# Kernel optimization log

Measured on AMD Instinct MI355X. Metric: run time of the kernel, lower is better.

The kernel has to match this reference:

```python
import jax, jax.numpy as jnp
import numpy as np

B, N, C, H = 2, 2048, 1024, 16
D = C // H  # head_dim = 64
EPS = 1e-6


def rmsnorm(x, w, eps=EPS):
    # RMSNorm over last dim (head_dim), matching torch RMSNorm (computed in fp32)
    x32 = x.astype(jnp.float32)
    y = x32 * jax.lax.rsqrt(jnp.mean(x32 * x32, axis=-1, keepdims=True) + eps)
    return y.astype(x.dtype) * w


def setup_inputs() -> dict:
    key = jax.random.key(0)
    ks = jax.random.split(key, 4)
    return {
        "x": jax.random.normal(ks[0], (B, N, C), dtype=jnp.float32),
        "w_qkv": jax.random.normal(ks[1], (C, 3 * C), dtype=jnp.float32) * 0.02,
        "b_qkv": jnp.zeros((3 * C,), dtype=jnp.float32),
        "q_w": jnp.ones((D,), dtype=jnp.float32),
        "k_w": jnp.ones((D,), dtype=jnp.float32),
        "w_proj": jax.random.normal(ks[2], (C, C), dtype=jnp.float32) * 0.02,
        "b_proj": jnp.zeros((C,), dtype=jnp.float32),
    }


def reference(x, w_qkv, b_qkv, q_w, k_w, w_proj, b_proj):
    b, n, c = x.shape
    h, d = H, c // H
    # QKV projection -> [3, B, H, N, D]
    qkv = (x @ w_qkv + b_qkv).reshape(b, n, 3, h, d).transpose(2, 0, 3, 1, 4)
    q, k, v = qkv[0], qkv[1], qkv[2]
    # per-head RMSNorm on q/k (qk_norm=True, use_rmsnorm=True)
    q = rmsnorm(q, q_w)
    k = rmsnorm(k, k_w)
    # scaled dot-product attention (scale = head_dim**-0.5, no dropout at eval)
    scale = d ** -0.5
    attn = jax.nn.softmax(jnp.einsum('bhqd,bhkd->bhqk', q, k) * scale, axis=-1)
    out = jnp.einsum('bhqk,bhkd->bhqd', attn, v)  # [B,H,N,D]
    out = out.transpose(0, 2, 1, 3).reshape(b, n, c)
    return out @ w_proj + b_proj
```

## Files before the change

### kernel.cpp

```cpp
#include <hip/hip_runtime.h>

typedef unsigned short u16;
typedef unsigned int u32;
typedef float f4 __attribute__((ext_vector_type(4)));
typedef __bf16 b8 __attribute__((ext_vector_type(8)));
typedef _Float16 h4 __attribute__((ext_vector_type(4)));
typedef _Float16 h8 __attribute__((ext_vector_type(8)));
typedef __fp16 hp2 __attribute__((ext_vector_type(2)));

#if __has_builtin(__builtin_amdgcn_exp2f)
#define EXP2(x) __builtin_amdgcn_exp2f(x)
#else
#define EXP2(x) exp2f(x)
#endif

__device__ __forceinline__ u16 f2bf(float f) {
  unsigned u = __float_as_uint(f);
  u += 0x7fffu + ((u >> 16) & 1u);
  return (u16)(u >> 16);
}
__device__ __forceinline__ float bf2f(u16 h) {
  return __uint_as_float(((unsigned)h) << 16);
}

__global__ void k_convert_all(const float* __restrict__ x,
                              const float* __restrict__ w_qkv,
                              const float* __restrict__ w_proj,
                              u16* __restrict__ xb, u16* __restrict__ wqkT,
                              u16* __restrict__ wpjT) {
  __shared__ u16 t[64][65];
  int bid = blockIdx.x;
  if (bid < 2048) {
    int i = (bid * 256 + threadIdx.x) * 8;
    float4 a = *(const float4*)(x + i);
    float4 b = *(const float4*)(x + i + 4);
    union { u16 h[8]; uint4 v; } r;
    r.h[0] = f2bf(a.x); r.h[1] = f2bf(a.y); r.h[2] = f2bf(a.z); r.h[3] = f2bf(a.w);
    r.h[4] = f2bf(b.x); r.h[5] = f2bf(b.y); r.h[6] = f2bf(b.z); r.h[7] = f2bf(b.w);
    *(uint4*)(xb + i) = r.v;
    return;
  }
  const float* w; u16* wT; int Ncols, Krows, bx, by;
  if (bid < 2816) { int l = bid - 2048; w = w_qkv; wT = wqkT; Ncols = 3072; Krows = 1024; bx = l % 48; by = l / 48; }
  else            { int l = bid - 2816; w = w_proj; wT = wpjT; Ncols = 1024; Krows = 1024; bx = l & 15; by = l >> 4; }
  int n0 = bx * 64, k0 = by * 64;
#pragma unroll
  for (int it = 0; it < 4; ++it) {
    int e = it * 256 + threadIdx.x;
    int r = e >> 4, c0 = (e & 15) * 4;
    float4 v = *(const float4*)(w + (size_t)(k0 + r) * Ncols + n0 + c0);
    t[r][c0] = f2bf(v.x); t[r][c0 + 1] = f2bf(v.y);
    t[r][c0 + 2] = f2bf(v.z); t[r][c0 + 3] = f2bf(v.w);
  }
  __syncthreads();
#pragma unroll
  for (int it = 0; it < 4; ++it) {
    int e = it * 256 + threadIdx.x;
    int r = e >> 4, c0 = (e & 15) * 4;
    union { u16 h[4]; uint2 v; } pk;
    pk.h[0] = t[c0][r]; pk.h[1] = t[c0 + 1][r];
    pk.h[2] = t[c0 + 2][r]; pk.h[3] = t[c0 + 3][r];
    *(uint2*)(wT + (size_t)(n0 + r) * Krows + k0 + c0) = pk.v;
  }
}

__global__ __launch_bounds__(512, 2) void k_gemm_qkv(
    const u16* __restrict__ A, const u16* __restrict__ Bt,
    const float* __restrict__ bias,
    u16* __restrict__ oq, u16* __restrict__ ok, u16* __restrict__ ov,
    const float* __restrict__ qw, const float* __restrict__ kw,
    int K) {
  __shared__ u16 lA[2][256 * 32];
  __shared__ u16 lB[2][256 * 32];
  const int tid = threadIdx.x;
  const int lane = tid & 63, lrow = lane & 15, lq = lane >> 4;
  const int wave = tid >> 6;
  const int bm = blockIdx.y * 256, bn = blockIdx.x * 256;
  const int wm = (wave >> 2) * 128;
  const int wn = (wave & 3) * 64;

  const int ch0 = tid, ch1 = 512 + tid;
  const u16* ap0 = A + (size_t)(bm + (ch0 >> 2)) * K + (ch0 & 3) * 8;
  const u16* ap1 = A + (size_t)(bm + (ch1 >> 2)) * K + (ch1 & 3) * 8;
  const u16* bp0 = Bt + (size_t)(bn + (ch0 >> 2)) * K + (ch0 & 3) * 8;
  const u16* bp1 = Bt + (size_t)(bn + (ch1 >> 2)) * K + (ch1 & 3) * 8;

  uint4 pA0 = *(const uint4*)ap0, pA1 = *(const uint4*)ap1;
  uint4 pB0 = *(const uint4*)bp0, pB1 = *(const uint4*)bp1;

  f4 acc[8][4] = {};
  const int iters = K >> 5;
  for (int it = 0; it < iters; ++it) {
    const int s = it & 1;
    *(uint4*)(lA[s] + ch0 * 8) = pA0; *(uint4*)(lA[s] + ch1 * 8) = pA1;
    *(uint4*)(lB[s] + ch0 * 8) = pB0; *(uint4*)(lB[s] + ch1 * 8) = pB1;
    if (it + 1 < iters) {
      ap0 += 32; ap1 += 32; bp0 += 32; bp1 += 32;
      pA0 = *(const uint4*)ap0; pA1 = *(const uint4*)ap1;
      pB0 = *(const uint4*)bp0; pB1 = *(const uint4*)bp1;
    }
    __syncthreads();
    b8 af[8], bf[4];
#pragma unroll
    for (int i = 0; i < 8; ++i)
      af[i] = *(const b8*)(lA[s] + (wm + i * 16 + lrow) * 32 + lq * 8);
#pragma unroll
    for (int j = 0; j < 4; ++j)
      bf[j] = *(const b8*)(lB[s] + (wn + j * 16 + lrow) * 32 + lq * 8);
#pragma unroll
    for (int i = 0; i < 8; ++i)
#pragma unroll
      for (int j = 0; j < 4; ++j)
        acc[i][j] = __builtin_amdgcn_mfma_f32_16x16x32_bf16(af[i], bf[j], acc[i][j], 0, 0, 0);
  }

  float bv[4];
#pragma unroll
  for (int j = 0; j < 4; ++j) bv[j] = bias[bn + wn + j * 16 + lrow];

  const float CS = 0.125f * 1.44269504088896340736f;
  const int n0w = bn + wn;
  const int sec = n0w >> 10;
  const int h = (n0w >> 6) & 15;
#pragma unroll
  for (int i = 0; i < 8; ++i) {
    float v[4][4];
#pragma unroll
    for (int j = 0; j < 4; ++j)
#pragma unroll
      for (int r = 0; r < 4; ++r) v[j][r] = acc[i][j][r] + bv[j];
    if (sec < 2) {
      u16* dst = sec == 0 ? oq : ok;
      const float* w = sec == 0 ? qw : kw;
      float ex = sec == 0 ? CS : 1.0f;
#pragma unroll
      for (int r = 0; r < 4; ++r) {
        float ss = v[0][r] * v[0][r] + v[1][r] * v[1][r] +
                   v[2][r] * v[2][r] + v[3][r] * v[3][r];
        ss += __shfl_xor(ss, 1, 64); ss += __shfl_xor(ss, 2, 64);
        ss += __shfl_xor(ss, 4, 64); ss += __shfl_xor(ss, 8, 64);
        float sc = rsqrtf(ss * (1.0f / 64.0f) + 1e-6f) * ex;
        int m = bm + wm + i * 16 + lq * 4 + r;
        int bb = m >> 11, ns = m & 2047;
        u16* rowp = dst + ((size_t)(bb * 16 + h) * 2048 + ns) * 64;
#pragma unroll
        for (int j = 0; j < 4; ++j) {
          int d = j * 16 + lrow;
          rowp[d] = f2bf(v[j][r] * sc * w[d]);
        }
      }
    } else {
      int m0 = bm + wm + i * 16 + lq * 4;
      int bb = m0 >> 11, ns = m0 & 2047;
#pragma unroll
      for (int j = 0; j < 4; ++j) {
        int d = j * 16 + lrow;
        union { _Float16 hh[4]; uint2 u; } pk;
#pragma unroll
        for (int r = 0; r < 4; ++r) pk.hh[r] = (_Float16)v[j][r];
        *(uint2*)(ov + ((size_t)(bb * 16 + h) * 64 + d) * 2048 + ns) = pk.u;
      }
    }
  }
}

__global__ __launch_bounds__(256, 4) void k_gemm2(
    const u16* __restrict__ A, const u16* __restrict__ Bt,
    const float* __restrict__ bias, float* __restrict__ outF,
    int K, int Ncols) {
  __shared__ u16 lA[2][64 * 32];
  __shared__ u16 lB[2][128 * 32];
  const int tid = threadIdx.x;
  const int lane = tid & 63, lrow = lane & 15, lq = lane >> 4;
  const int wave = tid >> 6;
  const int bm = blockIdx.y * 64, bn = blockIdx.x * 128;
  const int wm = (wave >> 1) * 32, wn = (wave & 1) * 64;

  const int cha = tid;
  const int ch0 = tid, ch1 = 256 + tid;
  const u16* ap = A + (size_t)(bm + (cha >> 2)) * K + (cha & 3) * 8;
  const u16* bp0 = Bt + (size_t)(bn + (ch0 >> 2)) * K + (ch0 & 3) * 8;
  const u16* bp1 = Bt + (size_t)(bn + (ch1 >> 2)) * K + (ch1 & 3) * 8;

  uint4 pA = *(const uint4*)ap;
  uint4 pB0 = *(const uint4*)bp0, pB1 = *(const uint4*)bp1;

  f4 acc[2][4] = {};
  const int iters = K >> 5;
  for (int it = 0; it < iters; ++it) {
    const int s = it & 1;
    *(uint4*)(lA[s] + cha * 8) = pA;
    *(uint4*)(lB[s] + ch0 * 8) = pB0; *(uint4*)(lB[s] + ch1 * 8) = pB1;
    if (it + 1 < iters) {
      ap += 32; bp0 += 32; bp1 += 32;
      pA = *(const uint4*)ap;
      pB0 = *(const uint4*)bp0; pB1 = *(const uint4*)bp1;
    }
    __syncthreads();
    b8 af[2], bf[4];
#pragma unroll
    for (int i = 0; i < 2; ++i)
      af[i] = *(const b8*)(lA[s] + (wm + i * 16 + lrow) * 32 + lq * 8);
#pragma unroll
    for (int j = 0; j < 4; ++j)
      bf[j] = *(const b8*)(lB[s] + (wn + j * 16 + lrow) * 32 + lq * 8);
#pragma unroll
    for (int i = 0; i < 2; ++i)
#pragma unroll
      for (int j = 0; j < 4; ++j)
        acc[i][j] = __builtin_amdgcn_mfma_f32_16x16x32_bf16(af[i], bf[j], acc[i][j], 0, 0, 0);
  }
#pragma unroll
  for (int i = 0; i < 2; ++i)
#pragma unroll
    for (int j = 0; j < 4; ++j) {
      int n = bn + wn + j * 16 + lrow;
      float bv = bias[n];
#pragma unroll
      for (int r = 0; r < 4; ++r) {
        int m = bm + wm + i * 16 + lq * 4 + r;
        outF[(size_t)m * Ncols + n] = acc[i][j][r] + bv;
      }
    }
}

__global__ __launch_bounds__(512, 2) void k_attn(
    const u16* __restrict__ qb, const u16* __restrict__ kb,
    const u16* __restrict__ vt, u16* __restrict__ ao) {
  __shared__ u16 lK[2][128 * 72];
  __shared__ u16 lV[2][64 * 140];
  const int b = blockIdx.x;
  const int bh = b & 31;
  const int q0 = (b >> 5) * 256;
  const int tid = threadIdx.x, wave = tid >> 6, lane = tid & 63;
  const int lrow = lane & 15, lq = lane >> 4;
  const int wq = wave * 32;

  b8 qf[2][2];
#pragma unroll
  for (int g = 0; g < 2; ++g)
#pragma unroll
    for (int ks = 0; ks < 2; ++ks)
      qf[g][ks] = *(const b8*)(qb + ((size_t)bh * 2048 + q0 + wq + g * 16 + lrow) * 64 +
                               ks * 32 + lq * 8);

  f4 o[2][4] = {};
  f4 lsum[2] = {};

  const int ch0 = tid, ch1 = 512 + tid;
  const u16* kp0 = kb + (size_t)bh * 2048 * 64 + (size_t)(ch0 >> 3) * 64 + (ch0 & 7) * 8;
  const u16* kp1 = kb + (size_t)bh * 2048 * 64 + (size_t)(ch1 >> 3) * 64 + (ch1 & 7) * 8;
  const u16* vp0 = vt + (size_t)bh * 64 * 2048 + (size_t)(ch0 >> 4) * 2048 + (ch0 & 15) * 8;
  const u16* vp1 = vt + (size_t)bh * 64 * 2048 + (size_t)(ch1 >> 4) * 2048 + (ch1 & 15) * 8;
  const int kO0 = (ch0 >> 3) * 72 + (ch0 & 7) * 8;
  const int kO1 = (ch1 >> 3) * 72 + (ch1 & 7) * 8;
  const int vO0 = (ch0 >> 4) * 140 + (ch0 & 15) * 8;
  const int vO1 = (ch1 >> 4) * 140 + (ch1 & 15) * 8;

  uint4 pK0 = *(const uint4*)kp0, pK1 = *(const uint4*)kp1;
  uint4 pV0 = *(const uint4*)vp0, pV1 = *(const uint4*)vp1;

  for (int it = 0; it < 16; ++it) {
    const int s = it & 1;
    *(uint4*)(lK[s] + kO0) = pK0;
    *(uint4*)(lK[s] + kO1) = pK1;
    *(uint2*)(lV[s] + vO0) = make_uint2(pV0.x, pV0.y);
    *(uint2*)(lV[s] + vO0 + 4) = make_uint2(pV0.z, pV0.w);
    *(uint2*)(lV[s] + vO1) = make_uint2(pV1.x, pV1.y);
    *(uint2*)(lV[s] + vO1 + 4) = make_uint2(pV1.z, pV1.w);

    if (it < 15) {
      kp0 += 128 * 64; kp1 += 128 * 64; vp0 += 128; vp1 += 128;
      pK0 = *(const uint4*)kp0; pK1 = *(const uint4*)kp1;
      pV0 = *(const uint4*)vp0; pV1 = *(const uint4*)vp1;
    }
    __syncthreads();

#pragma unroll
    for (int c = 0; c < 4; ++c) {
      f4 st[2][2] = {};
      __builtin_amdgcn_s_setprio(1);
#pragma unroll
      for (int ks = 0; ks < 2; ++ks)
#pragma unroll
        for (int t = 0; t < 2; ++t) {
          b8 kf = *(const b8*)(lK[s] + ((c * 2 + t) * 16 + lrow) * 72 + ks * 32 + lq * 8);
          st[0][t] = __builtin_amdgcn_mfma_f32_16x16x32_bf16(kf, qf[0][ks], st[0][t], 0, 0, 0);
          st[1][t] = __builtin_amdgcn_mfma_f32_16x16x32_bf16(kf, qf[1][ks], st[1][t], 0, 0, 0);
        }
      __builtin_amdgcn_s_setprio(0);

      h8 pf[2];
#pragma unroll
      for (int g = 0; g < 2; ++g) {
        f4 eA, eB;
#pragma unroll
        for (int r = 0; r < 4; ++r) eA[r] = EXP2(st[g][0][r]);
#pragma unroll
        for (int r = 0; r < 4; ++r) eB[r] = EXP2(st[g][1][r]);
        lsum[g] += eA;
        lsum[g] += eB;
        union { hp2 p2[4]; h8 v; } cv;
        cv.p2[0] = __builtin_amdgcn_cvt_pkrtz(eA[0], eA[1]);
        cv.p2[1] = __builtin_amdgcn_cvt_pkrtz(eA[2], eA[3]);
        cv.p2[2] = __builtin_amdgcn_cvt_pkrtz(eB[0], eB[1]);
        cv.p2[3] = __builtin_amdgcn_cvt_pkrtz(eB[2], eB[3]);
        pf[g] = cv.v;
      }

      __builtin_amdgcn_s_setprio(1);
#pragma unroll
      for (int dt = 0; dt < 4; ++dt) {
        const u16* vb = lV[s] + (dt * 16 + lrow) * 140 + c * 32 + lq * 4;
        union { h4 q[2]; h8 v; } va;
        va.q[0] = *(const h4*)vb;
        va.q[1] = *(const h4*)(vb + 16);
        o[0][dt] = __builtin_amdgcn_mfma_f32_16x16x32_f16(va.v, pf[0], o[0][dt], 0, 0, 0);
        o[1][dt] = __builtin_amdgcn_mfma_f32_16x16x32_f16(va.v, pf[1], o[1][dt], 0, 0, 0);
      }
      __builtin_amdgcn_s_setprio(0);
    }
  }

  const int bb = bh >> 4, h = bh & 15;
#pragma unroll
  for (int g = 0; g < 2; ++g) {
    float l = lsum[g][0] + lsum[g][1] + lsum[g][2] + lsum[g][3];
    l += __shfl_xor(l, 16, 64);
    l += __shfl_xor(l, 32, 64);
    float inv = 1.0f / l;
    int q = q0 + wq + g * 16 + lrow;
#pragma unroll
    for (int dt = 0; dt < 4; ++dt) {
      union { u16 h2[4]; uint2 v; } r;
#pragma unroll
      for (int rr = 0; rr < 4; ++rr) r.h2[rr] = f2bf(o[g][dt][rr] * inv);
      *(uint2*)(ao + ((size_t)bb * 2048 + q) * 1024 + h * 64 + dt * 16 + lq * 4) = r.v;
    }
  }
}

extern "C" void kernel_launch(void* const* d_in, const int* in_sizes, int n_in,
                              void* d_out, int out_size, void* d_ws, size_t ws_size,
                              hipStream_t stream) {
  const float* x      = (const float*)d_in[0];
  const float* w_qkv  = (const float*)d_in[1];
  const float* b_qkv  = (const float*)d_in[2];
  const float* q_w    = (const float*)d_in[3];
  const float* k_w    = (const float*)d_in[4];
  const float* w_proj = (const float*)d_in[5];
  const float* b_proj = (const float*)d_in[6];
  float* out = (float*)d_out;

  u16* xb   = (u16*)d_ws;
  u16* wqkT = xb + 4194304;
  u16* wpjT = wqkT + 3145728;
  u16* qb   = wpjT + 1048576;
  u16* kb   = qb + 4194304;
  u16* vtb  = kb + 4194304;
  u16* ao   = xb;

  k_convert_all<<<3072, 256, 0, stream>>>(x, w_qkv, w_proj, xb, wqkT, wpjT);
  k_gemm_qkv<<<dim3(12, 16), 512, 0, stream>>>(xb, wqkT, b_qkv, qb, kb, vtb, q_w, k_w, 1024);
  k_attn<<<256, 512, 0, stream>>>(qb, kb, vtb, ao);
  k_gemm2<<<dim3(8, 64), 256, 0, stream>>>(ao, wpjT, b_proj, out, 1024, 1024);
}
```

Baseline: 183.3 us.

## Fuse fp32-to-bf16 conversion and weight transpose into GEMM tile loads

Removes the separate conversion/transpose kernel. Both GEMMs now read fp32 activations and weights directly and convert to bf16 with v_cvt_pk_bf16_f32 while staging tiles into shared memory. Weights are read column-strided, 8 rows per thread, so the transpose happens in registers. The output-projection GEMM tile also grows from 64x128 to 128x128, with more accumulators per wave and a lower occupancy hint. This trades a kernel launch and an extra round trip through memory for strided scalar weight loads and twice the fp32 bytes per tile fetch, which could hurt load efficiency.

Result: slower. 209.8 us (+14.4%).

```diff
diff --git a/kernel.cpp b/kernel.cpp
--- a/kernel.cpp
+++ b/kernel.cpp
@@ -19,53 +19,15 @@
   u += 0x7fffu + ((u >> 16) & 1u);
   return (u16)(u >> 16);
 }
-__device__ __forceinline__ float bf2f(u16 h) {
-  return __uint_as_float(((unsigned)h) << 16);
-}
-
-__global__ void k_convert_all(const float* __restrict__ x,
-                              const float* __restrict__ w_qkv,
-                              const float* __restrict__ w_proj,
-                              u16* __restrict__ xb, u16* __restrict__ wqkT,
-                              u16* __restrict__ wpjT) {
-  __shared__ u16 t[64][65];
-  int bid = blockIdx.x;
-  if (bid < 2048) {
-    int i = (bid * 256 + threadIdx.x) * 8;
-    float4 a = *(const float4*)(x + i);
-    float4 b = *(const float4*)(x + i + 4);
-    union { u16 h[8]; uint4 v; } r;
-    r.h[0] = f2bf(a.x); r.h[1] = f2bf(a.y); r.h[2] = f2bf(a.z); r.h[3] = f2bf(a.w);
-    r.h[4] = f2bf(b.x); r.h[5] = f2bf(b.y); r.h[6] = f2bf(b.z); r.h[7] = f2bf(b.w);
-    *(uint4*)(xb + i) = r.v;
-    return;
-  }
-  const float* w; u16* wT; int Ncols, Krows, bx, by;
-  if (bid < 2816) { int l = bid - 2048; w = w_qkv; wT = wqkT; Ncols = 3072; Krows = 1024; bx = l % 48; by = l / 48; }
-  else            { int l = bid - 2816; w = w_proj; wT = wpjT; Ncols = 1024; Krows = 1024; bx = l & 15; by = l >> 4; }
-  int n0 = bx * 64, k0 = by * 64;
-#pragma unroll
-  for (int it = 0; it < 4; ++it) {
-    int e = it * 256 + threadIdx.x;
-    int r = e >> 4, c0 = (e & 15) * 4;
-    float4 v = *(const float4*)(w + (size_t)(k0 + r) * Ncols + n0 + c0);
-    t[r][c0] = f2bf(v.x); t[r][c0 + 1] = f2bf(v.y);
-    t[r][c0 + 2] = f2bf(v.z); t[r][c0 + 3] = f2bf(v.w);
-  }
-  __syncthreads();
-#pragma unroll
-  for (int it = 0; it < 4; ++it) {
-    int e = it * 256 + threadIdx.x;
-    int r = e >> 4, c0 = (e & 15) * 4;
-    union { u16 h[4]; uint2 v; } pk;
-    pk.h[0] = t[c0][r]; pk.h[1] = t[c0 + 1][r];
-    pk.h[2] = t[c0 + 2][r]; pk.h[3] = t[c0 + 3][r];
-    *(uint2*)(wT + (size_t)(n0 + r) * Krows + k0 + c0) = pk.v;
-  }
+
+__device__ __forceinline__ u32 pkbf(float lo, float hi) {
+  u32 r;
+  asm("v_cvt_pk_bf16_f32 %0, %1, %2" : "=v"(r) : "v"(lo), "v"(hi));
+  return r;
 }
 
 __global__ __launch_bounds__(512, 2) void k_gemm_qkv(
-    const u16* __restrict__ A, const u16* __restrict__ Bt,
+    const float* __restrict__ X, const float* __restrict__ W,
     const float* __restrict__ bias,
     u16* __restrict__ oq, u16* __restrict__ ok, u16* __restrict__ ov,
     const float* __restrict__ qw, const float* __restrict__ kw,
@@ -80,24 +42,47 @@
   const int wn = (wave & 3) * 64;
 
   const int ch0 = tid, ch1 = 512 + tid;
-  const u16* ap0 = A + (size_t)(bm + (ch0 >> 2)) * K + (ch0 & 3) * 8;
-  const u16* ap1 = A + (size_t)(bm + (ch1 >> 2)) * K + (ch1 & 3) * 8;
-  const u16* bp0 = Bt + (size_t)(bn + (ch0 >> 2)) * K + (ch0 & 3) * 8;
-  const u16* bp1 = Bt + (size_t)(bn + (ch1 >> 2)) * K + (ch1 & 3) * 8;
-
-  uint4 pA0 = *(const uint4*)ap0, pA1 = *(const uint4*)ap1;
-  uint4 pB0 = *(const uint4*)bp0, pB1 = *(const uint4*)bp1;
+  const float* xp0 = X + (size_t)(bm + (ch0 >> 2)) * K + (ch0 & 3) * 8;
+  const float* xp1 = X + (size_t)(bm + (ch1 >> 2)) * K + (ch1 & 3) * 8;
+  const int gB = tid & 3;
+  const float* wp0 = W + (size_t)(gB * 8) * 3072 + bn + (tid >> 2);
+  const float* wp1 = wp0 + 128;
+
+  float4 a0l = ((const float4*)xp0)[0], a0h = ((const float4*)xp0)[1];
+  float4 a1l = ((const float4*)xp1)[0], a1h = ((const float4*)xp1)[1];
+  float b0v[8], b1v[8];
+#pragma unroll
+  for (int kk = 0; kk < 8; ++kk) {
+    b0v[kk] = wp0[(size_t)kk * 3072];
+    b1v[kk] = wp1[(size_t)kk * 3072];
+  }
 
   f4 acc[8][4] = {};
   const int iters = K >> 5;
   for (int it = 0; it < iters; ++it) {
     const int s = it & 1;
-    *(uint4*)(lA[s] + ch0 * 8) = pA0; *(uint4*)(lA[s] + ch1 * 8) = pA1;
-    *(uint4*)(lB[s] + ch0 * 8) = pB0; *(uint4*)(lB[s] + ch1 * 8) = pB1;
+    uint4 r;
+    r.x = pkbf(a0l.x, a0l.y); r.y = pkbf(a0l.z, a0l.w);
+    r.z = pkbf(a0h.x, a0h.y); r.w = pkbf(a0h.z, a0h.w);
+    *(uint4*)(lA[s] + ch0 * 8) = r;
+    r.x = pkbf(a1l.x, a1l.y); r.y = pkbf(a1l.z, a1l.w);
+    r.z = pkbf(a1h.x, a1h.y); r.w = pkbf(a1h.z, a1h.w);
+    *(uint4*)(lA[s] + ch1 * 8) = r;
+    r.x = pkbf(b0v[0], b0v[1]); r.y = pkbf(b0v[2], b0v[3]);
+    r.z = pkbf(b0v[4], b0v[5]); r.w = pkbf(b0v[6], b0v[7]);
+    *(uint4*)(lB[s] + tid * 8) = r;
+    r.x = pkbf(b1v[0], b1v[1]); r.y = pkbf(b1v[2], b1v[3]);
+    r.z = pkbf(b1v[4], b1v[5]); r.w = pkbf(b1v[6], b1v[7]);
+    *(uint4*)(lB[s] + 4096 + tid * 8) = r;
     if (it + 1 < iters) {
-      ap0 += 32; ap1 += 32; bp0 += 32; bp1 += 32;
-      pA0 = *(const uint4*)ap0; pA1 = *(const uint4*)ap1;
-      pB0 = *(const uint4*)bp0; pB1 = *(const uint4*)bp1;
+      xp0 += 32; xp1 += 32; wp0 += 32 * 3072; wp1 += 32 * 3072;
+      a0l = ((const float4*)xp0)[0]; a0h = ((const float4*)xp0)[1];
+      a1l = ((const float4*)xp1)[0]; a1h = ((const float4*)xp1)[1];
+#pragma unroll
+      for (int kk = 0; kk < 8; ++kk) {
+        b0v[kk] = wp0[(size_t)kk * 3072];
+        b1v[kk] = wp1[(size_t)kk * 3072];
+      }
     }
     __syncthreads();
     b8 af[8], bf[4];
@@ -164,64 +149,80 @@
   }
 }
 
-__global__ __launch_bounds__(256, 4) void k_gemm2(
-    const u16* __restrict__ A, const u16* __restrict__ Bt,
+__global__ __launch_bounds__(256, 3) void k_gemm2(
+    const u16* __restrict__ A, const float* __restrict__ Wp,
     const float* __restrict__ bias, float* __restrict__ outF,
     int K, int Ncols) {
-  __shared__ u16 lA[2][64 * 32];
+  __shared__ u16 lA[2][128 * 32];
   __shared__ u16 lB[2][128 * 32];
   const int tid = threadIdx.x;
   const int lane = tid & 63, lrow = lane & 15, lq = lane >> 4;
   const int wave = tid >> 6;
-  const int bm = blockIdx.y * 64, bn = blockIdx.x * 128;
-  const int wm = (wave >> 1) * 32, wn = (wave & 1) * 64;
-
-  const int cha = tid;
+  const int bm = blockIdx.y * 128, bn = blockIdx.x * 128;
+  const int wm = (wave >> 1) * 64, wn = (wave & 1) * 64;
+
   const int ch0 = tid, ch1 = 256 + tid;
-  const u16* ap = A + (size_t)(bm + (cha >> 2)) * K + (cha & 3) * 8;
-  const u16* bp0 = Bt + (size_t)(bn + (ch0 >> 2)) * K + (ch0 & 3) * 8;
-  const u16* bp1 = Bt + (size_t)(bn + (ch1 >> 2)) * K + (ch1 & 3) * 8;
-
-  uint4 pA = *(const uint4*)ap;
-  uint4 pB0 = *(const uint4*)bp0, pB1 = *(const uint4*)bp1;
-
-  f4 acc[2][4] = {};
+  const u16* ap0 = A + (size_t)(bm + (ch0 >> 2)) * K + (ch0 & 3) * 8;
+  const u16* ap1 = A + (size_t)(bm + (ch1 >> 2)) * K + (ch1 & 3) * 8;
+  const int gB = tid & 3;
+  const float* wp0 = Wp + (size_t)(gB * 8) * 1024 + bn + (tid >> 2);
+  const float* wp1 = wp0 + 64;
+
+  uint4 pA0 = *(const uint4*)ap0, pA1 = *(const uint4*)ap1;
+  float b0v[8], b1v[8];
+#pragma unroll
+  for (int kk = 0; kk < 8; ++kk) {
+    b0v[kk] = wp0[(size_t)kk * 1024];
+    b1v[kk] = wp1[(size_t)kk * 1024];
+  }
+
+  f4 acc[4][4] = {};
   const int iters = K >> 5;
   for (int it = 0; it < iters; ++it) {
     const int s = it & 1;
-    *(uint4*)(lA[s] + cha * 8) = pA;
-    *(uint4*)(lB[s] + ch0 * 8) = pB0; *(uint4*)(lB[s] + ch1 * 8) = pB1;
+    *(uint4*)(lA[s] + ch0 * 8) = pA0; *(uint4*)(lA[s] + ch1 * 8) = pA1;
+    uint4 r;
+    r.x = pkbf(b0v[0], b0v[1]); r.y = pkbf(b0v[2], b0v[3]);
+    r.z = pkbf(b0v[4], b0v[5]); r.w = pkbf(b0v[6], b0v[7]);
+    *(uint4*)(lB[s] + tid * 8) = r;
+    r.x = pkbf(b1v[0], b1v[1]); r.y = pkbf(b1v[2], b1v[3]);
+    r.z = pkbf(b1v[4], b1v[5]); r.w = pkbf(b1v[6], b1v[7]);
+    *(uint4*)(lB[s] + 2048 + tid * 8) = r;
     if (it + 1 < iters) {
-      ap += 32; bp0 += 32; bp1 += 32;
-      pA = *(const uint4*)ap;
-      pB0 = *(const uint4*)bp0; pB1 = *(const uint4*)bp1;
+      ap0 += 32; ap1 += 32; wp0 += 32 * 1024; wp1 += 32 * 1024;
+      pA0 = *(const uint4*)ap0; pA1 = *(const uint4*)ap1;
+#pragma unroll
+      for (int kk = 0; kk < 8; ++kk) {
+        b0v[kk] = wp0[(size_t)kk * 1024];
+        b1v[kk] = wp1[(size_t)kk * 1024];
+      }
     }
     __syncthreads();
-    b8 af[2], bf[4];
-#pragma unroll
-    for (int i = 0; i < 2; ++i)
+    b8 af[4], bf[4];
+#pragma unroll
+    for (int i = 0; i < 4; ++i)
       af[i] = *(const b8*)(lA[s] + (wm + i * 16 + lrow) * 32 + lq * 8);
 #pragma unroll
     for (int j = 0; j < 4; ++j)
       bf[j] = *(const b8*)(lB[s] + (wn + j * 16 + lrow) * 32 + lq * 8);
 #pragma unroll
-    for (int i = 0; i < 2; ++i)
+    for (int i = 0; i < 4; ++i)
 #pragma unroll
       for (int j = 0; j < 4; ++j)
         acc[i][j] = __builtin_amdgcn_mfma_f32_16x16x32_bf16(af[i], bf[j], acc[i][j], 0, 0, 0);
   }
 #pragma unroll
-  for (int i = 0; i < 2; ++i)
-#pragma unroll
-    for (int j = 0; j < 4; ++j) {
-      int n = bn + wn + j * 16 + lrow;
-      float bv = bias[n];
+  for (int j = 0; j < 4; ++j) {
+    int n = bn + wn + j * 16 + lrow;
+    float bv = bias[n];
+#pragma unroll
+    for (int i = 0; i < 4; ++i)
 #pragma unroll
       for (int r = 0; r < 4; ++r) {
         int m = bm + wm + i * 16 + lq * 4 + r;
         outF[(size_t)m * Ncols + n] = acc[i][j][r] + bv;
       }
-    }
+  }
 }
 
 __global__ __launch_bounds__(512, 2) void k_attn(
@@ -352,16 +353,12 @@
   const float* b_proj = (const float*)d_in[6];
   float* out = (float*)d_out;
 
-  u16* xb   = (u16*)d_ws;
-  u16* wqkT = xb + 4194304;
-  u16* wpjT = wqkT + 3145728;
-  u16* qb   = wpjT + 1048576;
-  u16* kb   = qb + 4194304;
-  u16* vtb  = kb + 4194304;
-  u16* ao   = xb;
-
-  k_convert_all<<<3072, 256, 0, stream>>>(x, w_qkv, w_proj, xb, wqkT, wpjT);
-  k_gemm_qkv<<<dim3(12, 16), 512, 0, stream>>>(xb, wqkT, b_qkv, qb, kb, vtb, q_w, k_w, 1024);
+  u16* qb  = (u16*)d_ws;
+  u16* kb  = qb + 4194304;
+  u16* vtb = kb + 4194304;
+  u16* ao  = vtb + 4194304;
+
+  k_gemm_qkv<<<dim3(12, 16), 512, 0, stream>>>(x, w_qkv, b_qkv, qb, kb, vtb, q_w, k_w, 1024);
   k_attn<<<256, 512, 0, stream>>>(qb, kb, vtb, ao);
-  k_gemm2<<<dim3(8, 64), 256, 0, stream>>>(ao, wpjT, b_proj, out, 1024, 1024);
-}
+  k_gemm2<<<dim3(8, 32), 256, 0, stream>>>(ao, w_proj, b_proj, out, 1024, 1024);
+}
```
